# Kernel optimization log

Hardware: AMD Instinct MI355X
Metric: run time of the kernel (lower is better)

Reference implementation:

```python
import jax, jax.numpy as jnp
import numpy as np


def _neighbor_indices(H, W, r=10):
    # Faithful to init_neighbor_indices: for each pixel, the num_within_r nearest
    # pixels by Euclidean distance on the (H, W) grid (via argpartition).
    num = min(int(r * r * np.pi), H * W)  # 314 for r=10
    yy, xx = np.meshgrid(np.arange(H), np.arange(W), indexing='ij')
    fy, fx = yy.ravel(), xx.ravel()
    d2 = (fy[None, :] - fy[:, None]) ** 2 + (fx[None, :] - fx[:, None]) ** 2  # (I, I)
    idx = np.argpartition(d2, num, axis=1)[:, :num]  # (I, J)
    return idx.astype(np.int32)


def setup_inputs() -> dict:
    key = jax.random.key(0)
    ks = jax.random.split(key, 8)
    B, H, W, dim = 2, 48, 48, 64
    heads, dh, mult = 4, 8, 4
    inner = heads * dh            # 32
    hid = inner * mult // heads   # 32 per-head hidden channels
    n = H * W
    idx = jnp.asarray(_neighbor_indices(H, W, 10))
    s = lambda k, shp, sc: (jax.random.normal(k, shp, jnp.float32) * sc)
    return {
        'x': jax.random.normal(ks[0], (B, n, dim), jnp.float32),
        'idx': idx,                                   # (I, J) int32
        'w_qkv': s(ks[1], (dim, inner * 3), 0.08),    # Linear(dim, inner*3, bias=False)
        'w1': s(ks[2], (heads, hid, dh), 0.15),       # grouped 1x1 conv, per-head (out, in)
        'b1': s(ks[3], (heads, hid), 0.02),
        'w2': s(ks[4], (heads, dh, hid), 0.15),
        'b2': s(ks[5], (heads, dh), 0.02),
        'w_out': s(ks[6], (inner, dim), 0.1),         # Linear(inner, dim)
        'b_out': s(ks[7], (dim,), 0.02),
    }


def reference(x, idx, w_qkv, w1, b1, w2, b2, w_out, b_out):
    B, n, dim = x.shape
    h, hid, dh = w1.shape
    # qkv projection and head split: 'b n (h d) -> b h n d'
    q, k, v = jnp.split(x @ w_qkv, 3, axis=-1)
    sh = lambda t: t.reshape(B, n, h, dh).transpose(0, 2, 1, 3)  # (B,h,n,dh)
    q, k, v = sh(q), sh(k), sh(v)
    # neighbor gather (vector_select_batched_index): (B,h,I,J,dh)
    k1 = k[:, :, idx, :]
    v1 = v[:, :, idx, :]
    qk_rel = q[:, :, :, None, :] - k1                            # (B,h,I,J,dh)
    # attn_mlp: grouped 1x1 convs == per-head MLP over channel dim
    hmid = jax.nn.relu(jnp.einsum('bhijd,hed->bhije', qk_rel, w1)
                       + b1[None, :, None, None, :])
    sim = (jnp.einsum('bhije,hde->bhijd', hmid, w2)
           + b2[None, :, None, None, :])                        # (B,h,I,J,dh)
    # source softmaxes over dim=-2 of (B, h*dh, I, J), i.e. the pixel axis I
    attn = jax.nn.softmax(sim, axis=2)
    # einsum('b d i j, b i j d -> b i d') with channel d = (h dh)
    agg = jnp.einsum('bhijd,bhijd->bhid', attn, v1)              # (B,h,I,dh)
    agg = agg.transpose(0, 2, 1, 3).reshape(B, n, h * dh)
    return agg @ w_out + b_out
```

## Files before the change

kernel.cpp:

```cpp
#include <hip/hip_runtime.h>
#include <hip/hip_bf16.h>

#define BB 2
#define NH 4
#define NN 2304
#define DIM 64
#define DH 8
#define HID 32
#define KN 314

#define QKV_OFF 0
#define QKV_SZ  (BB*NN*96)
#define A_OFF   (QKV_OFF + QKV_SZ)
#define A_SZ    (BB*NH*NN*HID)
#define BK_OFF  (A_OFF + A_SZ)
#define BK_SZ   (BB*NH*NN*HID)
#define V_OFF   (BK_OFF + BK_SZ)
#define V_SZ    (BB*NH*NN*DH)
#define DEN_OFF (V_OFF + V_SZ)
#define DEN_SZ  (BB*NH*KN*DH)
#define AGG_OFF (DEN_OFF + DEN_SZ)
#define AGG_SZ  (BB*NH*NN*DH)
#define NUM_OFF (AGG_OFF + AGG_SZ)
#define NUM_ELTS ((size_t)BB*NH*NN*KN*DH)
#define BBF_OFF (NUM_OFF + NUM_ELTS/2)
#define WS_NEED_BYTES ((size_t)BBF_OFF*4 + (size_t)BK_SZ*2)

typedef float v2f __attribute__((ext_vector_type(2)));
typedef __attribute__((ext_vector_type(8))) short bf16x8;
typedef __attribute__((ext_vector_type(4))) float f32x4;
#define SWZ(x, imm) __int_as_float(__builtin_amdgcn_ds_swizzle(__float_as_int(x), imm))

static __device__ __forceinline__ float bfb(unsigned short u){
    return __uint_as_float(((unsigned)u) << 16);
}
static __device__ __forceinline__ unsigned cvtpk(float a, float b){
    unsigned r;
    asm("v_cvt_pk_bf16_f32 %0, %1, %2" : "=v"(r) : "v"(a), "v"(b));
    return r;
}
static __device__ __forceinline__ v2f unpk(unsigned u){
    v2f r; r.x = __uint_as_float(u << 16); r.y = __uint_as_float(u & 0xffff0000u); return r;
}
static __device__ __forceinline__ v2f mkv(float a, float b){ v2f r; r.x=a; r.y=b; return r; }

__global__ void qkv_kernel(const float* __restrict__ x, const float* __restrict__ w_qkv, float* ws){
    int t = blockIdx.x*256 + threadIdx.x;
    if (t >= BB*NN*96) return;
    int c = t % 96;
    int p = (t / 96) % NN;
    int b = t / (96*NN);
    const float* xr = x + (b*NN + p)*DIM;
    float acc = 0.f;
    #pragma unroll 8
    for (int dd=0; dd<DIM; dd++)
        acc = fmaf(xr[dd], w_qkv[dd*96 + c], acc);
    ws[QKV_OFF + (b*NN + p)*96 + c] = acc;
}

__global__ void ab_kernel(const float* __restrict__ w1, const float* __restrict__ b1, float* ws){
    int t = blockIdx.x*256 + threadIdx.x;
    if (t >= BB*NH*NN*HID) return;
    int e  = t % HID;
    int p  = (t / HID) % NN;
    int hh = (t / (HID*NN)) % NH;
    int b  = t / (HID*NN*NH);
    const float* qkv = ws + QKV_OFF + (b*NN + p)*96;
    const float* w1r = w1 + (hh*HID + e)*DH;
    float sa = b1[hh*HID + e];
    float sb = 0.f;
    #pragma unroll
    for (int d=0; d<DH; d++){
        float wv = w1r[d];
        sa = fmaf(wv, qkv[hh*DH + d],      sa);
        sb = fmaf(wv, qkv[32 + hh*DH + d], sb);
    }
    int base = ((b*NH + hh)*NN + p);
    ws[A_OFF  + base*HID + e] = sa;
    ws[BK_OFF + base*HID + e] = sb;
    ((unsigned short*)(ws + BBF_OFF))[(size_t)base*HID + e] = (unsigned short)cvtpk(sb, sb);
    if (e < DH)
        ws[V_OFF + base*DH + e] = qkv[64 + hh*DH + e];
}

__global__ __launch_bounds__(256) void pass1_mfma(const int* __restrict__ idx,
                                                  const float* __restrict__ w2,
                                                  const float* __restrict__ b2, float* ws){
    int lin = blockIdx.x + 20*(blockIdx.y + 12*blockIdx.z);
    int bh  = lin & 7;
    int rest = lin >> 3;
    int jt  = rest % 20;
    int yy  = rest / 20;
    int hh  = bh & (NH-1);
    int w = threadIdx.x >> 6, lane = threadIdx.x & 63;
    int n  = lane & 15;
    int kg = lane >> 4;
    int strip = yy*4 + w;
    int i0 = strip*48;

    const float LG2E = 1.44269504088896340736f;
    float wv[8];
    #pragma unroll
    for (int tt=0; tt<8; tt++)
        wv[tt] = (n < DH) ? w2[(hh*DH + n)*HID + kg*8 + tt]*LG2E : 0.f;
    union { unsigned u[4]; bf16x8 v; } bfr;
    bfr.u[0] = cvtpk(wv[0], wv[1]);
    bfr.u[1] = cvtpk(wv[2], wv[3]);
    bfr.u[2] = cvtpk(wv[4], wv[5]);
    bfr.u[3] = cvtpk(wv[6], wv[7]);
    f32x4 cinit;
    #pragma unroll
    for (int r=0; r<4; r++){
        int d = kg*4 + r;
        cinit[r] = (d < DH) ? b2[hh*DH + d]*LG2E : 0.f;
    }

    int jrow = jt*16 + n;
    int jj = jrow < KN ? jrow : (KN-1);
    bool stok = (jrow < KN) && (kg < 2);

    const float* Abuf = ws + A_OFF + (size_t)bh*NN*HID;
    const unsigned short* Bbf = (const unsigned short*)(ws + BBF_OFF) + (size_t)bh*NN*HID;
    const int* idxp = idx + (size_t)i0*KN + jj;
    const float* ap = Abuf + (size_t)i0*HID + kg*8;

    unsigned short* numb = (unsigned short*)(ws + NUM_OFF);
    size_t nb = (((size_t)bh*NN + i0)*KN + jj)*DH + kg*4;
    const size_t NPI = (size_t)KN*DH;

    f32x4 den; den[0]=0.f; den[1]=0.f; den[2]=0.f; den[3]=0.f;

    int p0 = idxp[0], p1 = idxp[KN]; idxp += 2*KN;
    uint4 Bc0 = *(const uint4*)(Bbf + (size_t)p0*HID + kg*8);
    uint4 Bc1 = *(const uint4*)(Bbf + (size_t)p1*HID + kg*8);
    p0 = idxp[0]; p1 = idxp[KN]; idxp += 2*KN;

    for (int ii=0; ii<48; ii+=2){
        float4 a00 = *(const float4*)ap;
        float4 a01 = *(const float4*)(ap+4);
        float4 a10 = *(const float4*)(ap+HID);
        float4 a11 = *(const float4*)(ap+HID+4);
        ap += 2*HID;

        uint4 Bn0 = Bc0, Bn1 = Bc1;
        if (ii < 46){
            Bn0 = *(const uint4*)(Bbf + (size_t)p0*HID + kg*8);
            Bn1 = *(const uint4*)(Bbf + (size_t)p1*HID + kg*8);
        }
        if (ii < 44){ p0 = idxp[0]; p1 = idxp[KN]; idxp += 2*KN; }

        v2f r;
        union { unsigned u[4]; bf16x8 v; } af0, af1;
        r = mkv(a00.x, a00.y) - unpk(Bc0.x);
        af0.u[0] = cvtpk(fmaxf(r.x,0.f), fmaxf(r.y,0.f));
        r = mkv(a00.z, a00.w) - unpk(Bc0.y);
        af0.u[1] = cvtpk(fmaxf(r.x,0.f), fmaxf(r.y,0.f));
        r = mkv(a01.x, a01.y) - unpk(Bc0.z);
        af0.u[2] = cvtpk(fmaxf(r.x,0.f), fmaxf(r.y,0.f));
        r = mkv(a01.z, a01.w) - unpk(Bc0.w);
        af0.u[3] = cvtpk(fmaxf(r.x,0.f), fmaxf(r.y,0.f));
        r = mkv(a10.x, a10.y) - unpk(Bc1.x);
        af1.u[0] = cvtpk(fmaxf(r.x,0.f), fmaxf(r.y,0.f));
        r = mkv(a10.z, a10.w) - unpk(Bc1.y);
        af1.u[1] = cvtpk(fmaxf(r.x,0.f), fmaxf(r.y,0.f));
        r = mkv(a11.x, a11.y) - unpk(Bc1.z);
        af1.u[2] = cvtpk(fmaxf(r.x,0.f), fmaxf(r.y,0.f));
        r = mkv(a11.z, a11.w) - unpk(Bc1.w);
        af1.u[3] = cvtpk(fmaxf(r.x,0.f), fmaxf(r.y,0.f));

        f32x4 d0 = __builtin_amdgcn_mfma_f32_16x16x32_bf16(bfr.v, af0.v, cinit, 0, 0, 0);
        f32x4 d1 = __builtin_amdgcn_mfma_f32_16x16x32_bf16(bfr.v, af1.v, cinit, 0, 0, 0);

        float e00 = exp2f(d0[0]), e01 = exp2f(d0[1]), e02 = exp2f(d0[2]), e03 = exp2f(d0[3]);
        float e10 = exp2f(d1[0]), e11 = exp2f(d1[1]), e12 = exp2f(d1[2]), e13 = exp2f(d1[3]);
        den[0] += e00 + e10; den[1] += e01 + e11;
        den[2] += e02 + e12; den[3] += e03 + e13;

        if (stok){
            uint2 s0; s0.x = cvtpk(e00, e01); s0.y = cvtpk(e02, e03);
            uint2 s1; s1.x = cvtpk(e10, e11); s1.y = cvtpk(e12, e13);
            *(uint2*)(numb + nb)       = s0;
            *(uint2*)(numb + nb + NPI) = s1;
        }
        nb += 2*NPI;

        Bc0 = Bn0; Bc1 = Bn1;
    }

    if (stok){
        float* denp = ws + DEN_OFF + ((size_t)bh*KN + jrow)*DH + kg*4;
        #pragma unroll
        for (int r2=0; r2<4; r2++)
            atomicAdd(denp + r2, den[r2]);
    }
}

__global__ void invden_kernel(float* ws){
    int t = blockIdx.x*256 + threadIdx.x;
    if (t < DEN_SZ){
        float* d = ws + DEN_OFF;
        d[t] = 1.0f / d[t];
    }
}

__global__ __launch_bounds__(256) void pass2f_kernel(const int* __restrict__ idx, float* ws){
    int hh = blockIdx.y, b = blockIdx.z;
    int w = threadIdx.x >> 6, lane = threadIdx.x & 63;
    int g = lane >> 3, dd = lane & 7;
    int bh = b*NH + hh;

    __shared__ float invs[KN*DH];
    {
        const float* den = ws + DEN_OFF + (size_t)bh*KN*DH;
        for (int t = threadIdx.x; t < KN*DH; t += 256) invs[t] = 1.0f / den[t];
    }
    __syncthreads();

    const float* Vbuf = ws + V_OFF + (size_t)bh*NN*DH;
    float* agg = ws + AGG_OFF + (size_t)bh*NN*DH;

    int i0 = blockIdx.x*8 + w*2;
    const unsigned short* num0 = (const unsigned short*)(ws + NUM_OFF)
                                 + ((size_t)bh*NN + i0)*KN*DH + dd;
    const unsigned short* num1 = num0 + (size_t)KN*DH;
    const int* ix0 = idx + (size_t)i0*KN;
    const int* ix1 = ix0 + KN;

    int p0 = ix0[g], p1 = ix1[g];
    float m0 = bfb(num0[g*DH]), m1 = bfb(num1[g*DH]);
    float acc0 = 0.f, acc1 = 0.f;

    for (int sg=0; sg<40; sg++){
        int jc = sg*8 + g;
        int jcc = jc < KN ? jc : (KN-1);
        float v0 = Vbuf[(size_t)p0*DH + dd];
        float v1 = Vbuf[(size_t)p1*DH + dd];
        float iv = invs[jcc*DH + dd];
        float w0 = m0 * iv, w1 = m1 * iv;
        if (jc >= KN){ w0 = 0.f; w1 = 0.f; }
        if (sg < 39){
            int jn = jc + 8; int jjn = jn < KN ? jn : (KN-1);
            p0 = ix0[jjn]; p1 = ix1[jjn];
            m0 = bfb(num0[(size_t)jjn*DH]);
            m1 = bfb(num1[(size_t)jjn*DH]);
        }
        acc0 = fmaf(w0, v0, acc0);
        acc1 = fmaf(w1, v1, acc1);
    }
    acc0 += __shfl_xor(acc0, 8, 64);
    acc0 += __shfl_xor(acc0, 16, 64);
    acc0 += __shfl_xor(acc0, 32, 64);
    acc1 += __shfl_xor(acc1, 8, 64);
    acc1 += __shfl_xor(acc1, 16, 64);
    acc1 += __shfl_xor(acc1, 32, 64);
    if (g == 0){
        agg[(size_t)i0*DH + dd]     = acc0;
        agg[(size_t)(i0+1)*DH + dd] = acc1;
    }
}

__device__ __forceinline__ void load_w2p(const float* __restrict__ w2, int hh, int dd,
                                         v2f w2a[8], v2f w2b[8]){
    #pragma unroll
    for (int m=0; m<8; m++){
        int d = dd ^ (((m&1)<<2) | (m&2) | ((m>>2)&1));
        const float* wp = w2 + (hh*DH + d)*HID + 4*dd;
        v2f a; a.x = wp[0]; a.y = wp[1];
        v2f b; b.x = wp[2]; b.y = wp[3];
        w2a[m] = a; w2b[m] = b;
    }
}
__device__ __forceinline__ float butterfly8p(float pr[8]){
    float q0 = pr[0] + SWZ(pr[4], 0x041F);
    float q1 = pr[1] + SWZ(pr[5], 0x041F);
    float q2 = pr[2] + SWZ(pr[6], 0x041F);
    float q3 = pr[3] + SWZ(pr[7], 0x041F);
    float r0 = q0 + SWZ(q2, 0x081F);
    float r1 = q1 + SWZ(q3, 0x081F);
    return r0 + SWZ(r1, 0x101F);
}
__global__ __launch_bounds__(256, 4) void pass1_small(const int* __restrict__ idx,
                                                      const float* __restrict__ w2,
                                                      const float* __restrict__ b2, float* ws){
    int sgic = blockIdx.x, hh = blockIdx.y, b = blockIdx.z;
    int sg = sgic >> 4, ic = sgic & 15;
    int w = threadIdx.x >> 6, lane = threadIdx.x & 63;
    int g = lane >> 3, dd = lane & 7;
    int j = sg*8 + g;
    bool jv = (j < KN);
    int jj = jv ? j : (KN-1);
    int bh = b*NH + hh;

    v2f w2a[8], w2b[8];
    load_w2p(w2, hh, dd, w2a, w2b);
    float b2v = b2[hh*DH + dd];

    const float* Abuf = ws + A_OFF  + (size_t)bh*NN*HID + 4*dd;
    const float* Bbuf = ws + BK_OFF + (size_t)bh*NN*HID + 4*dd;
    const int* idxc = idx + jj;

    float den_acc = 0.f;
    int i0 = ic*144 + w*36;
    for (int ii=0; ii<36; ii++){
        int i = i0 + ii;
        int p = idxc[(size_t)i*KN];
        float4 avv = *(const float4*)(Abuf + (size_t)i*HID);
        float4 bvv = *(const float4*)(Bbuf + (size_t)p*HID);
        v2f a0; a0.x=avv.x; a0.y=avv.y;
        v2f a1; a1.x=avv.z; a1.y=avv.w;
        v2f c0; c0.x=bvv.x; c0.y=bvv.y;
        v2f c1; c1.x=bvv.z; c1.y=bvv.w;
        v2f z;  z.x=0.f; z.y=0.f;
        v2f r0 = __builtin_elementwise_max(a0-c0, z);
        v2f r1 = __builtin_elementwise_max(a1-c1, z);
        float pr[8];
        #pragma unroll
        for (int m=0; m<8; m++){
            v2f t = w2a[m]*r0;
            t = __builtin_elementwise_fma(w2b[m], r1, t);
            pr[m] = t.x + t.y;
        }
        float sim = butterfly8p(pr) + b2v;
        den_acc += __expf(sim);
    }
    if (!jv) den_acc = 0.f;

    __shared__ float red[256];
    red[threadIdx.x] = den_acc;
    __syncthreads();
    if (w == 0 && jv){
        float s = red[lane] + red[lane+64] + red[lane+128] + red[lane+192];
        atomicAdd(ws + DEN_OFF + ((size_t)bh*KN + j)*DH + dd, s);
    }
}
__device__ __forceinline__ void load_w2s(const float* __restrict__ w2, int hh, int dd, float w2s[8][4]){
    #pragma unroll
    for (int m=0; m<8; m++){
        int d = ((m&1)<<2) | (m&2) | ((m>>2)&1);
        const float* wp = w2 + (hh*DH + d)*HID + 4*dd;
        w2s[m][0]=wp[0]; w2s[m][1]=wp[1]; w2s[m][2]=wp[2]; w2s[m][3]=wp[3];
    }
}
__device__ __forceinline__ float butterfly8(float pr[8], int dd){
    int b0 = dd&1, b1 = (dd>>1)&1, b2b = (dd>>2)&1;
    float q[4];
    #pragma unroll
    for (int t=0; t<4; t++){
        float send = pr[4*(1-b0)+t];
        float recv = __shfl_xor(send, 1, 64);
        q[t] = pr[4*b0+t] + recv;
    }
    float r[2];
    #pragma unroll
    for (int t=0; t<2; t++){
        float send = q[2*(1-b1)+t];
        float recv = __shfl_xor(send, 2, 64);
        r[t] = q[2*b1+t] + recv;
    }
    float send = r[1-b2b];
    float recv = __shfl_xor(send, 4, 64);
    return r[b2b] + recv;
}
__global__ __launch_bounds__(256) void pass2_kernel(const int* __restrict__ idx,
                                                    const float* __restrict__ w2,
                                                    const float* __restrict__ b2, float* ws){
    int ic = blockIdx.x, hh = blockIdx.y, b = blockIdx.z;
    int w = threadIdx.x >> 6, lane = threadIdx.x & 63;
    int g = lane >> 3, dd = lane & 7;

    float w2s[8][4];
    load_w2s(w2, hh, dd, w2s);
    float b2v = b2[hh*DH + dd];

    const float* Abuf = ws + A_OFF  + (size_t)(b*NH + hh)*NN*HID;
    const float* Bbuf = ws + BK_OFF + (size_t)(b*NH + hh)*NN*HID;
    const float* Vbuf = ws + V_OFF  + (size_t)(b*NH + hh)*NN*DH;
    const float* invd = ws + DEN_OFF + (size_t)(b*NH + hh)*KN*DH;
    float*       agg  = ws + AGG_OFF + (size_t)(b*NH + hh)*NN*DH;

    int i0 = ic*8 + w*2;
    #pragma unroll
    for (int ii=0; ii<2; ii++){
        int i = i0 + ii;
        float4 av = *(const float4*)(Abuf + (size_t)i*HID + 4*dd);
        float acc = 0.f;
        for (int sg=0; sg<40; sg++){
            int j = sg*8 + g;
            bool jvv = (j < KN);
            int jj = jvv ? j : (KN-1);
            int p = idx[i*KN + jj];
            float4 bv = *(const float4*)(Bbuf + (size_t)p*HID + 4*dd);
            float r0 = fmaxf(av.x-bv.x, 0.f), r1 = fmaxf(av.y-bv.y, 0.f);
            float r2 = fmaxf(av.z-bv.z, 0.f), r3 = fmaxf(av.w-bv.w, 0.f);
            float pr[8];
            #pragma unroll
            for (int m=0; m<8; m++)
                pr[m] = fmaf(w2s[m][0],r0, fmaf(w2s[m][1],r1, fmaf(w2s[m][2],r2, w2s[m][3]*r3)));
            float sim = butterfly8(pr, dd) + b2v;
            float attn = jvv ? (__expf(sim) * invd[(size_t)jj*DH + dd]) : 0.f;
            acc = fmaf(attn, Vbuf[(size_t)p*DH + dd], acc);
        }
        acc += __shfl_xor(acc, 8, 64);
        acc += __shfl_xor(acc, 16, 64);
        acc += __shfl_xor(acc, 32, 64);
        if (g == 0) agg[(size_t)i*DH + dd] = acc;
    }
}

__global__ void out_kernel(const float* __restrict__ w_out, const float* __restrict__ b_out,
                           const float* __restrict__ ws, float* __restrict__ out){
    int t = blockIdx.x*256 + threadIdx.x;
    if (t >= BB*NN*DIM) return;
    int c = t % DIM;
    int p = (t / DIM) % NN;
    int b = t / (DIM*NN);
    const float* agg = ws + AGG_OFF;
    float s = b_out[c];
    #pragma unroll
    for (int f=0; f<32; f++){
        int hh = f >> 3, d = f & 7;
        s = fmaf(agg[(((size_t)(b*NH + hh)*NN) + p)*DH + d], w_out[f*DIM + c], s);
    }
    out[t] = s;
}

extern "C" void kernel_launch(void* const* d_in, const int* in_sizes, int n_in,
                              void* d_out, int out_size, void* d_ws, size_t ws_size,
                              hipStream_t stream){
    const float* x     = (const float*)d_in[0];
    const int*   idx   = (const int*)d_in[1];
    const float* w_qkv = (const float*)d_in[2];
    const float* w1    = (const float*)d_in[3];
    const float* b1    = (const float*)d_in[4];
    const float* w2    = (const float*)d_in[5];
    const float* b2    = (const float*)d_in[6];
    const float* w_out = (const float*)d_in[7];
    const float* b_out = (const float*)d_in[8];
    float* ws  = (float*)d_ws;
    float* out = (float*)d_out;

    bool big = (ws_size >= WS_NEED_BYTES);

    hipMemsetAsync(ws + DEN_OFF, 0, DEN_SZ*sizeof(float), stream);

    qkv_kernel<<<(BB*NN*96 + 255)/256, 256, 0, stream>>>(x, w_qkv, ws);
    ab_kernel <<<(BB*NH*NN*HID + 255)/256, 256, 0, stream>>>(w1, b1, ws);
    if (big){
        pass1_mfma<<<dim3(20, 12, 8), 256, 0, stream>>>(idx, w2, b2, ws);
        pass2f_kernel<<<dim3(288, NH, BB), 256, 0, stream>>>(idx, ws);
    } else {
        pass1_small<<<dim3(640, NH, BB), 256, 0, stream>>>(idx, w2, b2, ws);
        invden_kernel<<<(DEN_SZ + 255)/256, 256, 0, stream>>>(ws);
        pass2_kernel<<<dim3(288, NH, BB), 256, 0, stream>>>(idx, w2, b2, ws);
    }
    out_kernel<<<(BB*NN*DIM + 255)/256, 256, 0, stream>>>(w_out, b_out, ws, out);
}
```

Measured before the change: 127.7 us.

## Switch pass1 hidden activations to fp16 packed math and deepen gather prefetch

Stores both the A (query-side) and B (key-side) hidden projections as fp16 in the workspace. pass1 now does the subtract and ReLU with packed half2 ops and feeds f16 MFMA instead of bf16, which replaces the float unpack/convert sequence and halves the A-operand load traffic. The neighbor-gather prefetch is also deepened from one to two iterations ahead. This changes numerics to fp16, which has finer mantissa than bf16 but a smaller range, and the deeper prefetch keeps more registers live.

```diff
diff --git a/kernel.cpp b/kernel.cpp
--- a/kernel.cpp
+++ b/kernel.cpp
@@ -23,13 +23,18 @@
 #define AGG_SZ  (BB*NH*NN*DH)
 #define NUM_OFF (AGG_OFF + AGG_SZ)
 #define NUM_ELTS ((size_t)BB*NH*NN*KN*DH)
-#define BBF_OFF (NUM_OFF + NUM_ELTS/2)
-#define WS_NEED_BYTES ((size_t)BBF_OFF*4 + (size_t)BK_SZ*2)
+#define BHF_OFF (NUM_OFF + NUM_ELTS/2)
+#define AHF_OFF (BHF_OFF + BK_SZ/2)
+#define WS_NEED_BYTES ((size_t)(AHF_OFF + A_SZ/2)*4)
 
 typedef float v2f __attribute__((ext_vector_type(2)));
 typedef __attribute__((ext_vector_type(8))) short bf16x8;
 typedef __attribute__((ext_vector_type(4))) float f32x4;
+typedef _Float16 fp16x8 __attribute__((ext_vector_type(8)));
+typedef _Float16 h2 __attribute__((ext_vector_type(2)));
 #define SWZ(x, imm) __int_as_float(__builtin_amdgcn_ds_swizzle(__float_as_int(x), imm))
+
+union U16x8 { uint4 q; h2 h[4]; fp16x8 v; };
 
 static __device__ __forceinline__ float bfb(unsigned short u){
     return __uint_as_float(((unsigned)u) << 16);
@@ -39,10 +44,10 @@
     asm("v_cvt_pk_bf16_f32 %0, %1, %2" : "=v"(r) : "v"(a), "v"(b));
     return r;
 }
-static __device__ __forceinline__ v2f unpk(unsigned u){
-    v2f r; r.x = __uint_as_float(u << 16); r.y = __uint_as_float(u & 0xffff0000u); return r;
-}
-static __device__ __forceinline__ v2f mkv(float a, float b){ v2f r; r.x=a; r.y=b; return r; }
+static __device__ __forceinline__ unsigned short f2h_bits(float f){
+    _Float16 h = (_Float16)f;
+    unsigned short u; __builtin_memcpy(&u, &h, 2); return u;
+}
 
 __global__ void qkv_kernel(const float* __restrict__ x, const float* __restrict__ w_qkv, float* ws){
     int t = blockIdx.x*256 + threadIdx.x;
@@ -78,7 +83,8 @@
     int base = ((b*NH + hh)*NN + p);
     ws[A_OFF  + base*HID + e] = sa;
     ws[BK_OFF + base*HID + e] = sb;
-    ((unsigned short*)(ws + BBF_OFF))[(size_t)base*HID + e] = (unsigned short)cvtpk(sb, sb);
+    ((unsigned short*)(ws + BHF_OFF))[(size_t)base*HID + e] = f2h_bits(sb);
+    ((unsigned short*)(ws + AHF_OFF))[(size_t)base*HID + e] = f2h_bits(sa);
     if (e < DH)
         ws[V_OFF + base*DH + e] = qkv[64 + hh*DH + e];
 }
@@ -99,15 +105,12 @@
     int i0 = strip*48;
 
     const float LG2E = 1.44269504088896340736f;
-    float wv[8];
-    #pragma unroll
-    for (int tt=0; tt<8; tt++)
-        wv[tt] = (n < DH) ? w2[(hh*DH + n)*HID + kg*8 + tt]*LG2E : 0.f;
-    union { unsigned u[4]; bf16x8 v; } bfr;
-    bfr.u[0] = cvtpk(wv[0], wv[1]);
-    bfr.u[1] = cvtpk(wv[2], wv[3]);
-    bfr.u[2] = cvtpk(wv[4], wv[5]);
-    bfr.u[3] = cvtpk(wv[6], wv[7]);
+    U16x8 bfr;
+    #pragma unroll
+    for (int tt=0; tt<8; tt++){
+        float wvv = (n < DH) ? w2[(hh*DH + n)*HID + kg*8 + tt]*LG2E : 0.f;
+        bfr.v[tt] = (_Float16)wvv;
+    }
     f32x4 cinit;
     #pragma unroll
     for (int r=0; r<4; r++){
@@ -119,57 +122,51 @@
     int jj = jrow < KN ? jrow : (KN-1);
     bool stok = (jrow < KN) && (kg < 2);
 
-    const float* Abuf = ws + A_OFF + (size_t)bh*NN*HID;
-    const unsigned short* Bbf = (const unsigned short*)(ws + BBF_OFF) + (size_t)bh*NN*HID;
+    const unsigned short* Ahf = (const unsigned short*)(ws + AHF_OFF) + (size_t)bh*NN*HID;
+    const unsigned short* Bhf = (const unsigned short*)(ws + BHF_OFF) + (size_t)bh*NN*HID;
     const int* idxp = idx + (size_t)i0*KN + jj;
-    const float* ap = Abuf + (size_t)i0*HID + kg*8;
+    const unsigned short* ap = Ahf + (size_t)i0*HID + kg*8;
 
     unsigned short* numb = (unsigned short*)(ws + NUM_OFF);
     size_t nb = (((size_t)bh*NN + i0)*KN + jj)*DH + kg*4;
     const size_t NPI = (size_t)KN*DH;
 
     f32x4 den; den[0]=0.f; den[1]=0.f; den[2]=0.f; den[3]=0.f;
+    const h2 zz = { (_Float16)0.f, (_Float16)0.f };
 
     int p0 = idxp[0], p1 = idxp[KN]; idxp += 2*KN;
-    uint4 Bc0 = *(const uint4*)(Bbf + (size_t)p0*HID + kg*8);
-    uint4 Bc1 = *(const uint4*)(Bbf + (size_t)p1*HID + kg*8);
+    uint4 Bc0 = *(const uint4*)(Bhf + (size_t)p0*HID + kg*8);
+    uint4 Bc1 = *(const uint4*)(Bhf + (size_t)p1*HID + kg*8);
     p0 = idxp[0]; p1 = idxp[KN]; idxp += 2*KN;
+    uint4 Bn0 = *(const uint4*)(Bhf + (size_t)p0*HID + kg*8);
+    uint4 Bn1 = *(const uint4*)(Bhf + (size_t)p1*HID + kg*8);
+    p0 = idxp[0]; p1 = idxp[KN]; idxp += 2*KN;
 
     for (int ii=0; ii<48; ii+=2){
-        float4 a00 = *(const float4*)ap;
-        float4 a01 = *(const float4*)(ap+4);
-        float4 a10 = *(const float4*)(ap+HID);
-        float4 a11 = *(const float4*)(ap+HID+4);
+        U16x8 Ah0, Ah1;
+        Ah0.q = *(const uint4*)ap;
+        Ah1.q = *(const uint4*)(ap + HID);
         ap += 2*HID;
 
-        uint4 Bn0 = Bc0, Bn1 = Bc1;
-        if (ii < 46){
-            Bn0 = *(const uint4*)(Bbf + (size_t)p0*HID + kg*8);
-            Bn1 = *(const uint4*)(Bbf + (size_t)p1*HID + kg*8);
-        }
-        if (ii < 44){ p0 = idxp[0]; p1 = idxp[KN]; idxp += 2*KN; }
-
-        v2f r;
-        union { unsigned u[4]; bf16x8 v; } af0, af1;
-        r = mkv(a00.x, a00.y) - unpk(Bc0.x);
-        af0.u[0] = cvtpk(fmaxf(r.x,0.f), fmaxf(r.y,0.f));
-        r = mkv(a00.z, a00.w) - unpk(Bc0.y);
-        af0.u[1] = cvtpk(fmaxf(r.x,0.f), fmaxf(r.y,0.f));
-        r = mkv(a01.x, a01.y) - unpk(Bc0.z);
-        af0.u[2] = cvtpk(fmaxf(r.x,0.f), fmaxf(r.y,0.f));
-        r = mkv(a01.z, a01.w) - unpk(Bc0.w);
-        af0.u[3] = cvtpk(fmaxf(r.x,0.f), fmaxf(r.y,0.f));
-        r = mkv(a10.x, a10.y) - unpk(Bc1.x);
-        af1.u[0] = cvtpk(fmaxf(r.x,0.f), fmaxf(r.y,0.f));
-        r = mkv(a10.z, a10.w) - unpk(Bc1.y);
-        af1.u[1] = cvtpk(fmaxf(r.x,0.f), fmaxf(r.y,0.f));
-        r = mkv(a11.x, a11.y) - unpk(Bc1.z);
-        af1.u[2] = cvtpk(fmaxf(r.x,0.f), fmaxf(r.y,0.f));
-        r = mkv(a11.z, a11.w) - unpk(Bc1.w);
-        af1.u[3] = cvtpk(fmaxf(r.x,0.f), fmaxf(r.y,0.f));
-
-        f32x4 d0 = __builtin_amdgcn_mfma_f32_16x16x32_bf16(bfr.v, af0.v, cinit, 0, 0, 0);
-        f32x4 d1 = __builtin_amdgcn_mfma_f32_16x16x32_bf16(bfr.v, af1.v, cinit, 0, 0, 0);
+        uint4 Bf0 = Bc0, Bf1 = Bc1;
+        if (ii < 44){
+            Bf0 = *(const uint4*)(Bhf + (size_t)p0*HID + kg*8);
+            Bf1 = *(const uint4*)(Bhf + (size_t)p1*HID + kg*8);
+        }
+        if (ii < 42){ p0 = idxp[0]; p1 = idxp[KN]; idxp += 2*KN; }
+
+        U16x8 Bu0, Bu1, af0, af1;
+        Bu0.q = Bc0; Bu1.q = Bc1;
+        #pragma unroll
+        for (int k=0; k<4; k++){
+            h2 d0h = Ah0.h[k] - Bu0.h[k];
+            af0.h[k] = __builtin_elementwise_max(d0h, zz);
+            h2 d1h = Ah1.h[k] - Bu1.h[k];
+            af1.h[k] = __builtin_elementwise_max(d1h, zz);
+        }
+
+        f32x4 d0 = __builtin_amdgcn_mfma_f32_16x16x32_f16(bfr.v, af0.v, cinit, 0, 0, 0);
+        f32x4 d1 = __builtin_amdgcn_mfma_f32_16x16x32_f16(bfr.v, af1.v, cinit, 0, 0, 0);
 
         float e00 = exp2f(d0[0]), e01 = exp2f(d0[1]), e02 = exp2f(d0[2]), e03 = exp2f(d0[3]);
         float e10 = exp2f(d1[0]), e11 = exp2f(d1[1]), e12 = exp2f(d1[2]), e13 = exp2f(d1[3]);
@@ -184,7 +181,7 @@
         }
         nb += 2*NPI;
 
-        Bc0 = Bn0; Bc1 = Bn1;
+        Bc0 = Bn0; Bc1 = Bn1; Bn0 = Bf0; Bn1 = Bf1;
     }
 
     if (stok){
```

New measurement: 119.9 us. 1.07x faster.
